# Kernel optimization log

Measured on AMD Instinct MI355X. Metric: run time of the kernel, lower is better.

Reference implementation:

```python
import jax, jax.numpy as jnp
import numpy as np

T, B, I, H = 512, 128, 512, 512

def setup_inputs() -> dict:
    key = jax.random.key(0)
    k1, k2, k3 = jax.random.split(key, 3)
    std = np.sqrt(1.0 / H).astype(np.float32)
    x = jax.random.normal(k1, (T, B, I), dtype=jnp.float32)
    w_ih = jax.random.normal(k2, (H, I), dtype=jnp.float32) * std
    w_hh = jax.random.normal(k3, (H, H), dtype=jnp.float32) * std
    b = jnp.zeros((H,), dtype=jnp.float32)
    return {"x": x, "w_ih": w_ih, "w_hh": w_hh, "b": b}

def reference(x, w_ih, w_hh, b):
    # Vanilla RNN: h_t = tanh(x_t @ W_ih^T + h_{t-1} @ W_hh^T + b)
    batch = x.shape[1]
    h0 = jnp.zeros((batch, w_hh.shape[0]), dtype=x.dtype)
    # Precompute the input projection for all timesteps in one GEMM.
    xw = jnp.einsum('tbi,hi->tbh', x, w_ih) + b  # [T,B,H]

    def step(h, xw_t):
        h_new = jnp.tanh(xw_t + h @ w_hh.T)
        return h_new, h_new

    h_final, outputs = jax.lax.scan(step, h0, xw)
    return outputs, h_final
```

## Files before the change

### kernel.cpp

```cpp
#include <hip/hip_runtime.h>

typedef _Float16 f16x8 __attribute__((ext_vector_type(8)));
typedef _Float16 f16x4 __attribute__((ext_vector_type(4)));
typedef float f32x4 __attribute__((ext_vector_type(4)));

#define TT 512
#define BB 128
#define II 512
#define HH 512
#define NBLK 32

__device__ __forceinline__ f16x8 cvt8(f32x4 a, f32x4 b) {
  f16x8 r;
  r[0] = (_Float16)a[0]; r[1] = (_Float16)a[1];
  r[2] = (_Float16)a[2]; r[3] = (_Float16)a[3];
  r[4] = (_Float16)b[0]; r[5] = (_Float16)b[1];
  r[6] = (_Float16)b[2]; r[7] = (_Float16)b[3];
  return r;
}

__global__ __launch_bounds__(256) void xw_gemm_f16(
    const float* __restrict__ X, const float* __restrict__ Wih,
    const float* __restrict__ bias, _Float16* __restrict__ out) {
  __shared__ _Float16 As[128][40];
  __shared__ _Float16 Bs[128][40];
  const int tid = threadIdx.x;
  const int lane = tid & 63, wv = tid >> 6;
  const int l15 = lane & 15, lhi = lane >> 4;
  const int ntile = blockIdx.x & 3;
  const int mtile = blockIdx.x >> 2;
  const int M0 = mtile * 128, N0 = ntile * 128;
  const int wm = (wv & 1) * 64, wn = (wv >> 1) * 64;

  f32x4 acc[4][4];
#pragma unroll
  for (int ni = 0; ni < 4; ++ni) {
    const float bv = bias[N0 + wn + ni * 16 + l15];
#pragma unroll
    for (int mi = 0; mi < 4; ++mi) {
      acc[mi][ni][0] = bv; acc[mi][ni][1] = bv;
      acc[mi][ni][2] = bv; acc[mi][ni][3] = bv;
    }
  }
  const int srow = tid >> 1;
  const int shalf = (tid & 1) * 16;

  for (int k0 = 0; k0 < II; k0 += 32) {
    const float* ax = X + (size_t)(M0 + srow) * II + k0 + shalf;
    const float* bx = Wih + (size_t)(N0 + srow) * II + k0 + shalf;
    f32x4 a0 = *(const f32x4*)ax,       a1 = *(const f32x4*)(ax + 4);
    f32x4 a2 = *(const f32x4*)(ax + 8), a3 = *(const f32x4*)(ax + 12);
    f32x4 b0 = *(const f32x4*)bx,       b1 = *(const f32x4*)(bx + 4);
    f32x4 b2 = *(const f32x4*)(bx + 8), b3 = *(const f32x4*)(bx + 12);
    *(f16x8*)&As[srow][shalf]     = cvt8(a0, a1);
    *(f16x8*)&As[srow][shalf + 8] = cvt8(a2, a3);
    *(f16x8*)&Bs[srow][shalf]     = cvt8(b0, b1);
    *(f16x8*)&Bs[srow][shalf + 8] = cvt8(b2, b3);
    __syncthreads();
    f16x8 af[4], bf[4];
#pragma unroll
    for (int mi = 0; mi < 4; ++mi) af[mi] = *(const f16x8*)&As[wm + mi * 16 + l15][lhi * 8];
#pragma unroll
    for (int ni = 0; ni < 4; ++ni) bf[ni] = *(const f16x8*)&Bs[wn + ni * 16 + l15][lhi * 8];
#pragma unroll
    for (int mi = 0; mi < 4; ++mi)
#pragma unroll
      for (int ni = 0; ni < 4; ++ni)
        acc[mi][ni] = __builtin_amdgcn_mfma_f32_16x16x32_f16(af[mi], bf[ni], acc[mi][ni], 0, 0, 0);
    __syncthreads();
  }
#pragma unroll
  for (int mi = 0; mi < 4; ++mi)
#pragma unroll
    for (int ni = 0; ni < 4; ++ni) {
      const int n = N0 + wn + ni * 16 + l15;
      const int bb = wm + mi * 16 + lhi * 4;
      f16x4 hv;
      hv[0] = (_Float16)acc[mi][ni][0]; hv[1] = (_Float16)acc[mi][ni][1];
      hv[2] = (_Float16)acc[mi][ni][2]; hv[3] = (_Float16)acc[mi][ni][3];
      *(f16x4*)&out[(((size_t)mtile * NBLK + (bb >> 2)) * HH + n) * 4] = hv;
    }
}

__global__ __launch_bounds__(512, 2) void rnn_rec_f16(
    const float* __restrict__ Whh,
    const _Float16* __restrict__ xw,
    float* __restrict__ hout) {
  __shared__ char lds[139264];
  char* wbase = lds;
  char* hb0 = lds + 131072;
  char* hb1 = lds + 135168;
  const int tid = threadIdx.x;
  const int lane = tid & 63, wv = tid >> 6;
  const int l15 = lane & 15, lhi = lane >> 4;
  const int blk = blockIdx.x;
  const int row0 = blk * 4;
  const int col0 = wv * 64;
  const int mycol = col0 + lhi * 16 + l15;

#pragma unroll
  for (int i = 0; i < 16; ++i) {
    const int u = i * 512 + tid;
    const int r = u >> 4;
    const int slot = u & 15;
    const float* src = Whh + (size_t)r * HH + 384 + slot * 8;
    *(f16x8*)(wbase + r * 256 + ((slot * 16) ^ ((r & 7) << 4))) =
        cvt8(*(const f32x4*)src, *(const f32x4*)(src + 4));
  }
  for (int i = tid; i < 1024; i += 512) ((unsigned int*)hb0)[i] = 0u;

  f16x8 wreg[48];
#pragma unroll
  for (int ni = 0; ni < 4; ++ni) {
    const float* wr = Whh + (size_t)(col0 + ni * 16 + l15) * HH + lhi * 8;
#pragma unroll
    for (int kj = 0; kj < 12; ++kj) {
      const float* s = wr + kj * 32;
      wreg[ni * 12 + kj] = cvt8(*(const f32x4*)s, *(const f32x4*)(s + 4));
    }
  }

  f16x4 pref = *(const f16x4*)&xw[((size_t)blk * HH + mycol) * 4];
  __syncthreads();

  const int arow = l15 & 3;
  const int arot = arow * 32;
  const int wcol2 = mycol * 2;

  for (int t = 0; t < TT; ++t) {
    char* rb = (t & 1) ? hb1 : hb0;
    char* wb = (t & 1) ? hb0 : hb1;
    f32x4 acc[4];
#pragma unroll
    for (int ni = 0; ni < 4; ++ni) {
      acc[ni][0] = 0.0f; acc[ni][1] = 0.0f; acc[ni][2] = 0.0f; acc[ni][3] = 0.0f;
    }
    const f16x4 myxw = pref;
    if (t + 1 < TT) {
      const size_t base = ((size_t)(t + 1) * NBLK + blk) * HH;
      pref = *(const f16x4*)&xw[(base + mycol) * 4];
    }
#pragma unroll
    for (int kj = 0; kj < 16; ++kj) {
      f16x8 af = *(const f16x8*)(rb + arow * 1024 + ((kj * 64 + lhi * 16 + arot) & 1023));
      if (kj < 12) {
#pragma unroll
        for (int ni = 0; ni < 4; ++ni)
          acc[ni] = __builtin_amdgcn_mfma_f32_16x16x32_f16(af, wreg[ni * 12 + kj], acc[ni], 0, 0, 0);
      } else {
#pragma unroll
        for (int ni = 0; ni < 4; ++ni) {
          const int wrow = col0 + ni * 16 + l15;
          f16x8 bf = *(const f16x8*)(wbase + wrow * 256 +
                        ((((kj - 12) * 32 + lhi * 8) * 2) ^ ((wrow & 7) << 4)));
          acc[ni] = __builtin_amdgcn_mfma_f32_16x16x32_f16(af, bf, acc[ni], 0, 0, 0);
        }
      }
    }
    float th4[4];
#pragma unroll
    for (int r = 0; r < 4; ++r) {
      const float s = (lhi == 0) ? acc[0][r]
                    : (lhi == 1) ? acc[1][r]
                    : (lhi == 2) ? acc[2][r]
                    :              acc[3][r];
      const float v = s + (float)myxw[r];
      const float xc = fminf(fmaxf(v, -4.97f), 4.97f);
      const float x2 = xc * xc;
      const float p = fmaf(x2, fmaf(x2, fmaf(x2, 1.0f, 378.0f), 17325.0f), 135135.0f) * xc;
      const float q = fmaf(x2, fmaf(x2, fmaf(x2, 28.0f, 3150.0f), 62370.0f), 135135.0f);
      const float th = p * __builtin_amdgcn_rcpf(q);
      th4[r] = th;
      *(_Float16*)(wb + r * 1024 + ((wcol2 + r * 32) & 1023)) = (_Float16)th;
    }
    {
      float* dst = hout + (size_t)t * (BB * HH) + (size_t)row0 * HH + mycol;
#pragma unroll
      for (int r = 0; r < 4; ++r)
        __builtin_nontemporal_store(th4[r], dst + (size_t)r * HH);
      if (t == TT - 1) {
        float* fdst = hout + (size_t)TT * (BB * HH) + (size_t)row0 * HH + mycol;
#pragma unroll
        for (int r = 0; r < 4; ++r)
          __builtin_nontemporal_store(th4[r], fdst + (size_t)r * HH);
      }
    }
    asm volatile("s_waitcnt lgkmcnt(0)" ::: "memory");
    __builtin_amdgcn_s_barrier();
    __builtin_amdgcn_sched_barrier(0);
  }
}

__global__ __launch_bounds__(256) void xw_gemm_f32(
    const float* __restrict__ X, const float* __restrict__ Wih,
    const float* __restrict__ bias, float* __restrict__ out) {
  __shared__ _Float16 As[128][40];
  __shared__ _Float16 Bs[128][40];
  const int tid = threadIdx.x;
  const int lane = tid & 63, wv = tid >> 6;
  const int l15 = lane & 15, lhi = lane >> 4;
  const int ntile = blockIdx.x & 3;
  const int mtile = blockIdx.x >> 2;
  const int M0 = mtile * 128, N0 = ntile * 128;
  const int wm = (wv & 1) * 64, wn = (wv >> 1) * 64;
  f32x4 acc[4][4];
#pragma unroll
  for (int ni = 0; ni < 4; ++ni) {
    const float bv = bias[N0 + wn + ni * 16 + l15];
#pragma unroll
    for (int mi = 0; mi < 4; ++mi) {
      acc[mi][ni][0] = bv; acc[mi][ni][1] = bv;
      acc[mi][ni][2] = bv; acc[mi][ni][3] = bv;
    }
  }
  const int srow = tid >> 1;
  const int shalf = (tid & 1) * 16;
  for (int k0 = 0; k0 < II; k0 += 32) {
    const float* ax = X + (size_t)(M0 + srow) * II + k0 + shalf;
    const float* bx = Wih + (size_t)(N0 + srow) * II + k0 + shalf;
    f32x4 a0 = *(const f32x4*)ax,       a1 = *(const f32x4*)(ax + 4);
    f32x4 a2 = *(const f32x4*)(ax + 8), a3 = *(const f32x4*)(ax + 12);
    f32x4 b0 = *(const f32x4*)bx,       b1 = *(const f32x4*)(bx + 4);
    f32x4 b2 = *(const f32x4*)(bx + 8), b3 = *(const f32x4*)(bx + 12);
    *(f16x8*)&As[srow][shalf]     = cvt8(a0, a1);
    *(f16x8*)&As[srow][shalf + 8] = cvt8(a2, a3);
    *(f16x8*)&Bs[srow][shalf]     = cvt8(b0, b1);
    *(f16x8*)&Bs[srow][shalf + 8] = cvt8(b2, b3);
    __syncthreads();
    f16x8 af[4], bf[4];
#pragma unroll
    for (int mi = 0; mi < 4; ++mi) af[mi] = *(const f16x8*)&As[wm + mi * 16 + l15][lhi * 8];
#pragma unroll
    for (int ni = 0; ni < 4; ++ni) bf[ni] = *(const f16x8*)&Bs[wn + ni * 16 + l15][lhi * 8];
#pragma unroll
    for (int mi = 0; mi < 4; ++mi)
#pragma unroll
      for (int ni = 0; ni < 4; ++ni)
        acc[mi][ni] = __builtin_amdgcn_mfma_f32_16x16x32_f16(af[mi], bf[ni], acc[mi][ni], 0, 0, 0);
    __syncthreads();
  }
#pragma unroll
  for (int mi = 0; mi < 4; ++mi)
#pragma unroll
    for (int ni = 0; ni < 4; ++ni) {
      const size_t rbase = (size_t)(M0 + wm + mi * 16 + lhi * 4) * HH + N0 + wn + ni * 16 + l15;
#pragma unroll
      for (int r = 0; r < 4; ++r) out[rbase + (size_t)r * HH] = acc[mi][ni][r];
    }
}

__global__ __launch_bounds__(512, 2) void rnn_rec_f32(
    const float* __restrict__ Whh,
    const float* __restrict__ xw,
    float* __restrict__ hout) {
  __shared__ char lds[163840];
  char* wbase = lds;
  char* hb0 = lds + 131072;
  char* hb1 = lds + 147456;
  const int tid = threadIdx.x;
  const int lane = tid & 63, wv = tid >> 6;
  const int l15 = lane & 15, lhi = lane >> 4;
  const int row0 = blockIdx.x * 16;
  const int col0 = wv * 64;
#pragma unroll
  for (int i = 0; i < 16; ++i) {
    const int u = i * 512 + tid;
    const int r = u >> 4;
    const int slot = u & 15;
    const float* src = Whh + (size_t)r * HH + 384 + slot * 8;
    *(f16x8*)(wbase + r * 256 + ((slot * 16) ^ ((r & 7) << 4))) =
        cvt8(*(const f32x4*)src, *(const f32x4*)(src + 4));
  }
  for (int i = tid; i < 4096; i += 512) ((unsigned int*)hb0)[i] = 0u;
  f16x8 wreg[48];
#pragma unroll
  for (int ni = 0; ni < 4; ++ni) {
    const float* wr = Whh + (size_t)(col0 + ni * 16 + l15) * HH + lhi * 8;
#pragma unroll
    for (int kj = 0; kj < 12; ++kj) {
      const float* s = wr + kj * 32;
      wreg[ni * 12 + kj] = cvt8(*(const f32x4*)s, *(const f32x4*)(s + 4));
    }
  }
  f32x4 pref[4];
  {
    const size_t base0 = (size_t)(row0 + lhi * 4) * HH + col0 + l15;
#pragma unroll
    for (int ni = 0; ni < 4; ++ni)
#pragma unroll
      for (int r = 0; r < 4; ++r)
        pref[ni][r] = xw[base0 + (size_t)r * HH + ni * 16];
  }
  __syncthreads();
  const int fa = ((l15 & 7) ^ ((l15 >> 3) << 1)) << 4;
  for (int t = 0; t < TT; ++t) {
    char* rb = (t & 1) ? hb1 : hb0;
    char* wb = (t & 1) ? hb0 : hb1;
    f32x4 acc[4];
#pragma unroll
    for (int ni = 0; ni < 4; ++ni) acc[ni] = pref[ni];
    if (t + 1 < TT) {
      const size_t base = (size_t)(t + 1) * (BB * HH) + (size_t)(row0 + lhi * 4) * HH + col0 + l15;
#pragma unroll
      for (int ni = 0; ni < 4; ++ni)
#pragma unroll
        for (int r = 0; r < 4; ++r)
          pref[ni][r] = xw[base + (size_t)r * HH + ni * 16];
    }
#pragma unroll
    for (int kj = 0; kj < 12; ++kj) {
      f16x8 af = *(const f16x8*)(rb + l15 * 1024 + ((kj * 64 + lhi * 16) ^ fa));
#pragma unroll
      for (int ni = 0; ni < 4; ++ni)
        acc[ni] = __builtin_amdgcn_mfma_f32_16x16x32_f16(af, wreg[ni * 12 + kj], acc[ni], 0, 0, 0);
    }
#pragma unroll
    for (int kj = 12; kj < 16; ++kj) {
      f16x8 af = *(const f16x8*)(rb + l15 * 1024 + ((kj * 64 + lhi * 16) ^ fa));
#pragma unroll
      for (int ni = 0; ni < 4; ++ni) {
        const int wrow = col0 + ni * 16 + l15;
        f16x8 bf = *(const f16x8*)(wbase + wrow * 256 +
                      ((((kj - 12) * 32 + lhi * 8) * 2) ^ ((wrow & 7) << 4)));
        acc[ni] = __builtin_amdgcn_mfma_f32_16x16x32_f16(af, bf, acc[ni], 0, 0, 0);
      }
    }
#pragma unroll
    for (int ni = 0; ni < 4; ++ni)
#pragma unroll
      for (int r = 0; r < 4; ++r) {
        const float v = acc[ni][r];
        const float xc = fminf(fmaxf(v, -4.97f), 4.97f);
        const float x2 = xc * xc;
        const float p = fmaf(x2, fmaf(x2, fmaf(x2, 1.0f, 378.0f), 17325.0f), 135135.0f) * xc;
        const float q = fmaf(x2, fmaf(x2, fmaf(x2, 28.0f, 3150.0f), 62370.0f), 135135.0f);
        const float th = p * __builtin_amdgcn_rcpf(q);
        const int hrow = lhi * 4 + r;
        const int fw = ((hrow & 7) ^ ((hrow >> 3) << 1)) << 4;
        *(_Float16*)(wb + hrow * 1024 +
                     (((col0 + ni * 16 + l15) * 2) ^ fw)) = (_Float16)th;
      }
    asm volatile("s_waitcnt lgkmcnt(0)" ::: "memory");
    __builtin_amdgcn_s_barrier();
    __builtin_amdgcn_sched_barrier(0);
#pragma unroll
    for (int q = 0; q < 2; ++q) {
      const int hrow = wv * 2 + q;
      const int fw = ((hrow & 7) ^ ((hrow >> 3) << 1)) << 4;
      f16x8 hv = *(const f16x8*)(wb + hrow * 1024 + ((lane * 16) ^ fw));
      f32x4 lo, hi;
      lo[0] = (float)hv[0]; lo[1] = (float)hv[1]; lo[2] = (float)hv[2]; lo[3] = (float)hv[3];
      hi[0] = (float)hv[4]; hi[1] = (float)hv[5]; hi[2] = (float)hv[6]; hi[3] = (float)hv[7];
      float* dst = hout + (size_t)t * (BB * HH) + (size_t)(row0 + hrow) * HH + lane * 8;
      *(f32x4*)dst = lo;
      *(f32x4*)(dst + 4) = hi;
      if (t == TT - 1) {
        float* fdst = hout + (size_t)TT * (BB * HH) + (size_t)(row0 + hrow) * HH + lane * 8;
        *(f32x4*)fdst = lo;
        *(f32x4*)(fdst + 4) = hi;
      }
    }
  }
}

extern "C" void kernel_launch(void* const* d_in, const int* in_sizes, int n_in,
                              void* d_out, int out_size, void* d_ws, size_t ws_size,
                              hipStream_t stream) {
  (void)in_sizes; (void)n_in; (void)out_size;
  const float* x    = (const float*)d_in[0];
  const float* w_ih = (const float*)d_in[1];
  const float* w_hh = (const float*)d_in[2];
  const float* b    = (const float*)d_in[3];
  float* out = (float*)d_out;
  const size_t need = (size_t)TT * HH * BB * sizeof(_Float16);
  if (ws_size >= need) {
    _Float16* xwbuf = (_Float16*)d_ws;
    xw_gemm_f16<<<dim3(2048), dim3(256), 0, stream>>>(x, w_ih, b, xwbuf);
    rnn_rec_f16<<<dim3(NBLK), dim3(512), 0, stream>>>(w_hh, xwbuf, out);
  } else {
    xw_gemm_f32<<<dim3(2048), dim3(256), 0, stream>>>(x, w_ih, b, out);
    rnn_rec_f32<<<dim3(8), dim3(512), 0, stream>>>(w_hh, out, out);
  }
}
```

Measured before the change: 961.1 us.

## Halve recurrence block to 4 waves, each computing 128 hidden columns

The recurrent kernel now runs with 256 threads (4 waves) per block instead of 512, and each wave covers 128 output columns using 8 MFMA column tiles instead of 4. This doubles the register-resident W_hh slice per wave (96 f16x8 registers) and handles two xw prefetches and two tanh/store halves per lane. The goal is to cut per-step barrier cost across fewer waves and reuse each LDS A-fragment load across more MFMAs. The cost is much higher register pressure with a risk of spills, and fewer waves to hide latency on the serial critical path.

```diff
diff --git a/kernel.cpp b/kernel.cpp
--- a/kernel.cpp
+++ b/kernel.cpp
@@ -82,7 +82,7 @@
     }
 }
 
-__global__ __launch_bounds__(512, 2) void rnn_rec_f16(
+__global__ __launch_bounds__(256, 1) void rnn_rec_f16(
     const float* __restrict__ Whh,
     const _Float16* __restrict__ xw,
     float* __restrict__ hout) {
@@ -95,23 +95,23 @@
   const int l15 = lane & 15, lhi = lane >> 4;
   const int blk = blockIdx.x;
   const int row0 = blk * 4;
-  const int col0 = wv * 64;
+  const int col0 = wv * 128;
   const int mycol = col0 + lhi * 16 + l15;
 
 #pragma unroll
-  for (int i = 0; i < 16; ++i) {
-    const int u = i * 512 + tid;
+  for (int i = 0; i < 32; ++i) {
+    const int u = i * 256 + tid;
     const int r = u >> 4;
     const int slot = u & 15;
     const float* src = Whh + (size_t)r * HH + 384 + slot * 8;
     *(f16x8*)(wbase + r * 256 + ((slot * 16) ^ ((r & 7) << 4))) =
         cvt8(*(const f32x4*)src, *(const f32x4*)(src + 4));
   }
-  for (int i = tid; i < 1024; i += 512) ((unsigned int*)hb0)[i] = 0u;
-
-  f16x8 wreg[48];
-#pragma unroll
-  for (int ni = 0; ni < 4; ++ni) {
+  for (int i = tid; i < 1024; i += 256) ((unsigned int*)hb0)[i] = 0u;
+
+  f16x8 wreg[96];
+#pragma unroll
+  for (int ni = 0; ni < 8; ++ni) {
     const float* wr = Whh + (size_t)(col0 + ni * 16 + l15) * HH + lhi * 8;
 #pragma unroll
     for (int kj = 0; kj < 12; ++kj) {
@@ -120,36 +120,38 @@
     }
   }
 
-  f16x4 pref = *(const f16x4*)&xw[((size_t)blk * HH + mycol) * 4];
+  f16x4 prefA = *(const f16x4*)&xw[((size_t)blk * HH + mycol) * 4];
+  f16x4 prefB = *(const f16x4*)&xw[((size_t)blk * HH + mycol + 64) * 4];
   __syncthreads();
 
   const int arow = l15 & 3;
   const int arot = arow * 32;
-  const int wcol2 = mycol * 2;
 
   for (int t = 0; t < TT; ++t) {
     char* rb = (t & 1) ? hb1 : hb0;
     char* wb = (t & 1) ? hb0 : hb1;
-    f32x4 acc[4];
-#pragma unroll
-    for (int ni = 0; ni < 4; ++ni) {
+    f32x4 acc[8];
+#pragma unroll
+    for (int ni = 0; ni < 8; ++ni) {
       acc[ni][0] = 0.0f; acc[ni][1] = 0.0f; acc[ni][2] = 0.0f; acc[ni][3] = 0.0f;
     }
-    const f16x4 myxw = pref;
+    const f16x4 myxwA = prefA;
+    const f16x4 myxwB = prefB;
     if (t + 1 < TT) {
       const size_t base = ((size_t)(t + 1) * NBLK + blk) * HH;
-      pref = *(const f16x4*)&xw[(base + mycol) * 4];
+      prefA = *(const f16x4*)&xw[(base + mycol) * 4];
+      prefB = *(const f16x4*)&xw[(base + mycol + 64) * 4];
     }
 #pragma unroll
     for (int kj = 0; kj < 16; ++kj) {
       f16x8 af = *(const f16x8*)(rb + arow * 1024 + ((kj * 64 + lhi * 16 + arot) & 1023));
       if (kj < 12) {
 #pragma unroll
-        for (int ni = 0; ni < 4; ++ni)
+        for (int ni = 0; ni < 8; ++ni)
           acc[ni] = __builtin_amdgcn_mfma_f32_16x16x32_f16(af, wreg[ni * 12 + kj], acc[ni], 0, 0, 0);
       } else {
 #pragma unroll
-        for (int ni = 0; ni < 4; ++ni) {
+        for (int ni = 0; ni < 8; ++ni) {
           const int wrow = col0 + ni * 16 + l15;
           f16x8 bf = *(const f16x8*)(wbase + wrow * 256 +
                         ((((kj - 12) * 32 + lhi * 8) * 2) ^ ((wrow & 7) << 4)));
@@ -157,32 +159,41 @@
         }
       }
     }
-    float th4[4];
-#pragma unroll
-    for (int r = 0; r < 4; ++r) {
-      const float s = (lhi == 0) ? acc[0][r]
-                    : (lhi == 1) ? acc[1][r]
-                    : (lhi == 2) ? acc[2][r]
-                    :              acc[3][r];
-      const float v = s + (float)myxw[r];
-      const float xc = fminf(fmaxf(v, -4.97f), 4.97f);
-      const float x2 = xc * xc;
-      const float p = fmaf(x2, fmaf(x2, fmaf(x2, 1.0f, 378.0f), 17325.0f), 135135.0f) * xc;
-      const float q = fmaf(x2, fmaf(x2, fmaf(x2, 28.0f, 3150.0f), 62370.0f), 135135.0f);
-      const float th = p * __builtin_amdgcn_rcpf(q);
-      th4[r] = th;
-      *(_Float16*)(wb + r * 1024 + ((wcol2 + r * 32) & 1023)) = (_Float16)th;
+    float th4[2][4];
+#pragma unroll
+    for (int half = 0; half < 2; ++half) {
+      const int wcol2 = (mycol + half * 64) * 2;
+#pragma unroll
+      for (int r = 0; r < 4; ++r) {
+        const float s = (lhi == 0) ? acc[half * 4 + 0][r]
+                      : (lhi == 1) ? acc[half * 4 + 1][r]
+                      : (lhi == 2) ? acc[half * 4 + 2][r]
+                      :              acc[half * 4 + 3][r];
+        const float xwv = half ? (float)myxwB[r] : (float)myxwA[r];
+        const float v = s + xwv;
+        const float xc = fminf(fmaxf(v, -4.97f), 4.97f);
+        const float x2 = xc * xc;
+        const float p = fmaf(x2, fmaf(x2, fmaf(x2, 1.0f, 378.0f), 17325.0f), 135135.0f) * xc;
+        const float q = fmaf(x2, fmaf(x2, fmaf(x2, 28.0f, 3150.0f), 62370.0f), 135135.0f);
+        const float th = p * __builtin_amdgcn_rcpf(q);
+        th4[half][r] = th;
+        *(_Float16*)(wb + r * 1024 + ((wcol2 + r * 32) & 1023)) = (_Float16)th;
+      }
     }
     {
       float* dst = hout + (size_t)t * (BB * HH) + (size_t)row0 * HH + mycol;
 #pragma unroll
-      for (int r = 0; r < 4; ++r)
-        __builtin_nontemporal_store(th4[r], dst + (size_t)r * HH);
+      for (int half = 0; half < 2; ++half)
+#pragma unroll
+        for (int r = 0; r < 4; ++r)
+          __builtin_nontemporal_store(th4[half][r], dst + (size_t)r * HH + half * 64);
       if (t == TT - 1) {
         float* fdst = hout + (size_t)TT * (BB * HH) + (size_t)row0 * HH + mycol;
 #pragma unroll
-        for (int r = 0; r < 4; ++r)
-          __builtin_nontemporal_store(th4[r], fdst + (size_t)r * HH);
+        for (int half = 0; half < 2; ++half)
+#pragma unroll
+          for (int r = 0; r < 4; ++r)
+            __builtin_nontemporal_store(th4[half][r], fdst + (size_t)r * HH + half * 64);
       }
     }
     asm volatile("s_waitcnt lgkmcnt(0)" ::: "memory");
@@ -376,7 +387,7 @@
   if (ws_size >= need) {
     _Float16* xwbuf = (_Float16*)d_ws;
     xw_gemm_f16<<<dim3(2048), dim3(256), 0, stream>>>(x, w_ih, b, xwbuf);
-    rnn_rec_f16<<<dim3(NBLK), dim3(512), 0, stream>>>(w_hh, xwbuf, out);
+    rnn_rec_f16<<<dim3(NBLK), dim3(256), 0, stream>>>(w_hh, xwbuf, out);
   } else {
     xw_gemm_f32<<<dim3(2048), dim3(256), 0, stream>>>(x, w_ih, b, out);
     rnn_rec_f32<<<dim3(8), dim3(512), 0, stream>>>(w_hh, out, out);
```

New measurement: 1.555 ms. 61.8% more time.
